# Performance work log

Hardware: AMD Instinct MI355X
Metric: run time of the kernel (lower is better)

## Reference

```python
import jax, jax.numpy as jnp
import numpy as np

EPS = 1e-5      # numerical floor for degrees / std / attenuation
LEAK = 0.01     # LeakyReLU slope of mixing FCLayer
AVG_D = 3.3     # log(avg_degree + 1) from init_kwargs
BIG = 1e30      # masking constant for max/min aggregators


def setup_inputs() -> dict:
    key = jax.random.key(0)
    ks = jax.random.split(key, 12)
    B, N, Din, De, H = 8, 256, 128, 64, 128
    s = 0.05
    inp = {
        "input": jax.random.normal(ks[0], (B, N, Din), jnp.float32),
        "adj": (jax.random.uniform(ks[1], (B, N, N)) < 0.1).astype(jnp.float32),
        "adj_features": jax.random.normal(ks[2], (B, N, N, De), jnp.float32),
        "hidden": jnp.zeros((B * N, H), jnp.float32),
        "pre_W": jax.random.normal(ks[3], (2 * Din + De, Din), jnp.float32) * s,
        "pre_b": jnp.zeros((Din,), jnp.float32),
        "post_W": jax.random.normal(ks[4], (13 * Din, H), jnp.float32) * s,
        "post_b": jnp.zeros((H,), jnp.float32),
        "mix_W": jax.random.normal(ks[5], (H, H), jnp.float32) * s,
        "mix_b": jnp.zeros((H,), jnp.float32),
        "gru_Wih": jax.random.normal(ks[6], (3 * H, H), jnp.float32) * s,
        "gru_Whh": jax.random.normal(ks[7], (3 * H, H), jnp.float32) * s,
    }
    return inp


def reference(input, adj, adj_features, hidden, pre_W, pre_b, post_W, post_b,
              mix_W, mix_b, gru_Wih, gru_Whh):
    B, N, Din = input.shape
    H = mix_W.shape[1]
    # --- pretrans MLP over all pairs: Linear([h_i, h_j, e_ij]) ---
    # split the weight into blocks so we never materialize h_cat (B,N,N,2Din+De)
    Wi, Wj, We = pre_W[:Din], pre_W[Din:2 * Din], pre_W[2 * Din:]
    hi = input @ Wi            # (B,N,Din)
    hj = input @ Wj            # (B,N,Din)
    h_mod = (hi[:, :, None, :] + hj[:, None, :, :]
             + jnp.einsum('bije,ek->bijk', adj_features, We) + pre_b)  # (B,N,N,Din)
    # --- multi-aggregator masked reduction over source axis j ---
    deg = jnp.sum(adj, axis=2)                       # (B,N)
    degc = jnp.maximum(deg, EPS)[..., None]          # (B,N,1)
    s1 = jnp.einsum('bij,bijk->bik', adj, h_mod)
    s2 = jnp.einsum('bij,bijk->bik', adj, h_mod * h_mod)
    mean = s1 / degc
    var = jnp.maximum(s2 / degc - mean * mean, 0.0)
    std = jnp.sqrt(var + EPS)
    mask = adj[..., None] > 0
    has_nb = (deg > 0)[..., None]
    mx = jnp.where(has_nb, jnp.max(jnp.where(mask, h_mod, -BIG), axis=2), 0.0)
    mn = jnp.where(has_nb, jnp.min(jnp.where(mask, h_mod, BIG), axis=2), 0.0)
    m = jnp.concatenate([mean, mx, mn, std], axis=2)  # (B,N,4*Din)
    # --- scalers: identity, amplification, attenuation ---
    slog = (jnp.log(deg + 1.0) / AVG_D)[..., None]    # (B,N,1)
    m = jnp.concatenate([m, m * slog, m / (slog + EPS)], axis=2)  # (B,N,12*Din)
    # --- posttrans Linear + mixing FCLayer (LeakyReLU) ---
    m_cat = jnp.concatenate([input, m], axis=2)       # (B,N,13*Din)
    y = m_cat @ post_W + post_b                       # (B,N,H)
    y = y @ mix_W + mix_b
    y = jnp.where(y > 0, y, LEAK * y)
    # --- GRUCell (bias=False), torch gate order r,z,n ---
    x = y.reshape(B * N, H)
    gi = x @ gru_Wih.T
    gh = hidden @ gru_Whh.T
    r = jax.nn.sigmoid(gi[:, :H] + gh[:, :H])
    z = jax.nn.sigmoid(gi[:, H:2 * H] + gh[:, H:2 * H])
    n = jnp.tanh(gi[:, 2 * H:] + r * gh[:, 2 * H:])
    h_new = (1.0 - z) * n + z * hidden
    return h_new.reshape(B, N, H)
```

## Files before the change

### kernel.cpp

```cpp
#include <hip/hip_runtime.h>
#include <cstdint>
#include <cstddef>

#define EPSF 1e-5f
#define LEAKF 0.01f
#define AVGD 3.3f

static constexpr int Nn = 256, DIN = 128, DE = 64, Hn = 128;
static constexpr int BN = 2048;
static constexpr int KP = 1664;
static constexpr int KM = 1536;

typedef short bf16x8 __attribute__((ext_vector_type(8)));
typedef float f32x4  __attribute__((ext_vector_type(4)));
union BF8 { bf16x8 v; uint16_t u[8]; };

__device__ __forceinline__ float bf2f(uint16_t u) { return __uint_as_float(((uint32_t)u) << 16); }
__device__ __forceinline__ float bflo(uint32_t u)  { return __uint_as_float(u << 16); }
__device__ __forceinline__ uint16_t f2bf(float f) {
  uint32_t u = __float_as_uint(f);
  u += 0x7fffu + ((u >> 16) & 1u);
  return (uint16_t)(u >> 16);
}

__device__ __forceinline__ int detect_bf16(const uint32_t* w) {
  float lo = bflo(w[threadIdx.x & 63]);
  unsigned long long ok = __ballot(fabsf(lo) < 64.f);
  return ok == 0xFFFFFFFFFFFFFFFFull;
}
__device__ __forceinline__ float loadf(const void* p, size_t i, int isbf) {
  return isbf ? bf2f(((const uint16_t*)p)[i]) : ((const float*)p)[i];
}
__device__ __forceinline__ bf16x8 load_a8(const void* p, size_t elem, int isbf) {
  if (isbf) return *(const bf16x8*)((const uint16_t*)p + elem);
  const float* s = (const float*)p + elem;
  BF8 r;
  #pragma unroll
  for (int e = 0; e < 8; e++) r.u[e] = f2bf(s[e]);
  return r.v;
}
__device__ __forceinline__ f32x4 mfma16(bf16x8 a, bf16x8 b, f32x4 c) {
  return __builtin_amdgcn_mfma_f32_16x16x32_bf16(a, b, c, 0, 0, 0);
}

__global__ __launch_bounds__(256) void k_prep1(
    const void* __restrict__ input, const void* __restrict__ pre_W,
    const void* __restrict__ pre_b, const void* __restrict__ post_W,
    const void* __restrict__ mix_W, const void* __restrict__ Wih,
    const void* __restrict__ Whh,
    uint16_t* __restrict__ postTb, uint16_t* __restrict__ mixTb,
    uint16_t* __restrict__ WeB, uint16_t* __restrict__ Wihb,
    uint16_t* __restrict__ Whhb,
    float* __restrict__ hi, float* __restrict__ hj) {
  __shared__ float tile[32][33];
  int isbf = detect_bf16((const uint32_t*)input);
  int b = blockIdx.x, tid = threadIdx.x;

  if (b >= 276) {
    int lane = tid & 63, w = tid >> 6;
    int wg = (b - 276) * 4 + w;
    int rt = wg >> 4, nt = wg & 15;
    int ishj = nt >> 3, ct = nt & 7;
    int m16 = lane & 15, quad = lane >> 4;
    int col = ct * 16 + m16;
    int row = rt * 16 + m16;
    int kbase = ishj ? 128 : 0;
    f32x4 acc = {0.f, 0.f, 0.f, 0.f};
    #pragma unroll
    for (int kt = 0; kt < 4; kt++) {
      bf16x8 a = load_a8(input, (size_t)row * 128 + kt * 32 + quad * 8, isbf);
      BF8 bb;
      #pragma unroll
      for (int j = 0; j < 8; j++)
        bb.u[j] = f2bf(loadf(pre_W, (size_t)(kbase + kt * 32 + quad * 8 + j) * 128 + col, isbf));
      acc = mfma16(a, bb.v, acc);
    }
    float bias = ishj ? 0.f : loadf(pre_b, col, isbf);
    float* dst = ishj ? hj : hi;
    #pragma unroll
    for (int r = 0; r < 4; r++)
      dst[(size_t)(rt * 16 + quad * 4 + r) * 128 + col] = acc[r] + bias;
    return;
  }

  if (b < 224) {
    const void* src; uint16_t* bdst; int R, t;
    if (b < 208) { src = post_W; bdst = postTb; R = KP;  t = b; }
    else         { src = mix_W;  bdst = mixTb;  R = 128; t = b - 208; }
    int bx = t & 3, by = t >> 2;
    int tx = tid & 31, ty = tid >> 5;
    int c0 = bx * 32, r0 = by * 32;
    #pragma unroll
    for (int dy = 0; dy < 32; dy += 8)
      tile[ty + dy][tx] = loadf(src, (size_t)(r0 + ty + dy) * 128 + (c0 + tx), isbf);
    __syncthreads();
    #pragma unroll
    for (int dy = 0; dy < 32; dy += 8)
      bdst[(size_t)(c0 + ty + dy) * R + (r0 + tx)] = f2bf(tile[tx][ty + dy]);
  } else {
    const void* src; uint16_t* dst; int base; size_t soff = 0;
    if (b < 228)      { src = pre_W; dst = WeB;  base = (b - 224) * 2048; soff = 256 * 128; }
    else if (b < 252) { src = Wih;   dst = Wihb; base = (b - 228) * 2048; }
    else              { src = Whh;   dst = Whhb; base = (b - 252) * 2048; }
    int i = base + tid * 8;
    uint16_t v[8];
    if (isbf) *(uint4*)v = *(const uint4*)((const uint16_t*)src + soff + i);
    else { const float* s = (const float*)src + soff + i;
           #pragma unroll
           for (int e = 0; e < 8; e++) v[e] = f2bf(s[e]); }
    *(uint4*)(dst + i) = *(uint4*)v;
  }
}

__global__ __launch_bounds__(256) void k2_mfma(
    const void* __restrict__ input, const void* __restrict__ adj_raw,
    const void* __restrict__ af_raw,
    const float* __restrict__ hi, const float* __restrict__ hj,
    const uint16_t* __restrict__ WeB, uint16_t* __restrict__ Mb) {
  __shared__ int s_cnt;
  __shared__ int nbr[Nn];
  __shared__ __align__(16) uint16_t A_lds[2][16 * 72];
  int isbf = detect_bf16((const uint32_t*)input);
  int bi = blockIdx.x, tid = threadIdx.x;
  if (tid == 0) s_cnt = 0;
  __syncthreads();
  {
    float a = loadf(adj_raw, (size_t)bi * Nn + tid, isbf);
    if (a > 0.f) nbr[atomicAdd(&s_cnt, 1)] = tid;
  }
  __syncthreads();
  int cnt = s_cnt;

  int lane = tid & 63, w = tid >> 6;
  int m16 = lane & 15, quad = lane >> 4;
  int col0 = w * 32 + m16, col1 = col0 + 16;

  BF8 b00, b01, b10, b11;
  #pragma unroll
  for (int j = 0; j < 8; j++) {
    int k0 = quad * 8 + j, k1 = k0 + 32;
    b00.u[j] = WeB[(size_t)k0 * 128 + col0];
    b01.u[j] = WeB[(size_t)k1 * 128 + col0];
    b10.u[j] = WeB[(size_t)k0 * 128 + col1];
    b11.u[j] = WeB[(size_t)k1 * 128 + col1];
  }
  float base0 = hi[(size_t)bi * 128 + col0];
  float base1 = hi[(size_t)bi * 128 + col1];
  const float* hjb = &hj[(size_t)(bi & ~(Nn - 1)) * 128];

  float s1a = 0.f, s2a = 0.f, mxa = -1e30f, mna = 1e30f;
  float s1b = 0.f, s2b = 0.f, mxb = -1e30f, mnb = 1e30f;

  auto stage = [&](int ce, int buf) {
    if (tid < 128) {
      int e = tid >> 3, seg = tid & 7;
      int ei = ce + e; if (ei >= cnt) ei = cnt - 1;
      int j = nbr[ei];
      uint16_t v[8];
      if (isbf)
        *(uint4*)v = *(const uint4*)((const uint16_t*)af_raw + ((size_t)bi * Nn + j) * DE + seg * 8);
      else {
        const float* s = (const float*)af_raw + ((size_t)bi * Nn + j) * DE + seg * 8;
        #pragma unroll
        for (int x = 0; x < 8; x++) v[x] = f2bf(s[x]);
      }
      *(uint4*)&A_lds[buf][e * 72 + seg * 8] = *(uint4*)v;
    }
  };

  if (cnt > 0) stage(0, 0);
  __syncthreads();

  for (int ce = 0; ce < cnt; ce += 16) {
    int cur = (ce >> 4) & 1;
    if (ce + 16 < cnt) stage(ce + 16, cur ^ 1);
    float hjv0[4], hjv1[4]; int vld[4];
    #pragma unroll
    for (int r = 0; r < 4; r++) {
      int e = ce + quad * 4 + r;
      vld[r] = (e < cnt);
      int j = nbr[vld[r] ? e : (cnt - 1)];
      hjv0[r] = hjb[(size_t)j * 128 + col0];
      hjv1[r] = hjb[(size_t)j * 128 + col1];
    }
    bf16x8 a0 = *(const bf16x8*)&A_lds[cur][m16 * 72 + quad * 8];
    bf16x8 a1 = *(const bf16x8*)&A_lds[cur][m16 * 72 + 32 + quad * 8];
    f32x4 C0 = {0.f,0.f,0.f,0.f}, C1 = C0;
    C0 = mfma16(a0, b00.v, C0); C0 = mfma16(a1, b01.v, C0);
    C1 = mfma16(a0, b10.v, C1); C1 = mfma16(a1, b11.v, C1);
    #pragma unroll
    for (int r = 0; r < 4; r++) {
      float h0 = base0 + hjv0[r] + C0[r];
      float h1 = base1 + hjv1[r] + C1[r];
      if (vld[r]) {
        s1a += h0; s2a += h0 * h0; mxa = fmaxf(mxa, h0); mna = fminf(mna, h0);
        s1b += h1; s2b += h1 * h1; mxb = fmaxf(mxb, h1); mnb = fminf(mnb, h1);
      }
    }
    __syncthreads();
  }

  #pragma unroll
  for (int off = 16; off <= 32; off <<= 1) {
    s1a += __shfl_xor(s1a, off); s2a += __shfl_xor(s2a, off);
    mxa = fmaxf(mxa, __shfl_xor(mxa, off)); mna = fminf(mna, __shfl_xor(mna, off));
    s1b += __shfl_xor(s1b, off); s2b += __shfl_xor(s2b, off);
    mxb = fmaxf(mxb, __shfl_xor(mxb, off)); mnb = fminf(mnb, __shfl_xor(mnb, off));
  }
  if (quad == 0) {
    float deg = (float)cnt, degc = fmaxf(deg, EPSF);
    float slog = logf(deg + 1.f) / AVGD;
    float inv  = 1.f / (slog + EPSF);
    uint16_t* mo = Mb + (size_t)bi * KM;
    #pragma unroll
    for (int t = 0; t < 2; t++) {
      float s1 = t ? s1b : s1a, s2 = t ? s2b : s2a;
      float mx = t ? mxb : mxa, mn = t ? mnb : mna;
      int col = t ? col1 : col0;
      float mean = s1 / degc;
      float var  = fmaxf(s2 / degc - mean * mean, 0.f);
      float stdv = sqrtf(var + EPSF);
      if (cnt == 0) { mx = 0.f; mn = 0.f; }
      mo[0*128+col]  = f2bf(mean);        mo[1*128+col]  = f2bf(mx);
      mo[2*128+col]  = f2bf(mn);          mo[3*128+col]  = f2bf(stdv);
      mo[4*128+col]  = f2bf(mean * slog); mo[5*128+col]  = f2bf(mx * slog);
      mo[6*128+col]  = f2bf(mn * slog);   mo[7*128+col]  = f2bf(stdv * slog);
      mo[8*128+col]  = f2bf(mean * inv);  mo[9*128+col]  = f2bf(mx * inv);
      mo[10*128+col] = f2bf(mn * inv);    mo[11*128+col] = f2bf(stdv * inv);
    }
  }
}

__global__ __launch_bounds__(512) void k3_fused(
    const void* __restrict__ input, const uint16_t* __restrict__ Mb,
    const uint16_t* __restrict__ postTb, const void* __restrict__ post_b,
    const uint16_t* __restrict__ mixTb, const void* __restrict__ mix_b,
    const uint16_t* __restrict__ Wihb, const uint16_t* __restrict__ Whhb,
    const void* __restrict__ hidden, void* __restrict__ out) {
  constexpr int SX = 136;
  __shared__ __align__(16) uint16_t y_s[16 * SX];
  __shared__ __align__(16) uint16_t x_s[16 * SX];
  __shared__ __align__(16) uint16_t hid_s[16 * SX];
  int isbf = detect_bf16((const uint32_t*)input);
  int tid = threadIdx.x;
  int n0 = blockIdx.x * 16;
  if (tid < 256) {
    int row = tid >> 4, c = (tid & 15) * 8;
    uint16_t v[8];
    if (isbf) *(uint4*)v = *(const uint4*)((const uint16_t*)hidden + (size_t)(n0 + row) * 128 + c);
    else { const float* s = (const float*)hidden + (size_t)(n0 + row) * 128 + c;
           #pragma unroll
           for (int e = 0; e < 8; e++) v[e] = f2bf(s[e]); }
    *(uint4*)&hid_s[row * SX + c] = *(uint4*)v;
  }
  int lane = tid & 63, w = tid >> 6;
  int m16 = lane & 15, quad = lane >> 4;
  int col = w * 16 + m16;

  f32x4 acc0 = {0.f,0.f,0.f,0.f}, acc1 = acc0;
  const uint16_t* bp = postTb + (size_t)col * KP + quad * 8;
  #pragma unroll
  for (int kt = 0; kt < 4; kt += 2) {
    bf16x8 a0 = load_a8(input, (size_t)(n0 + m16) * 128 + kt * 32 + quad * 8, isbf);
    bf16x8 a1 = load_a8(input, (size_t)(n0 + m16) * 128 + kt * 32 + 32 + quad * 8, isbf);
    acc0 = mfma16(a0, *(const bf16x8*)(bp + kt * 32), acc0);
    acc1 = mfma16(a1, *(const bf16x8*)(bp + kt * 32 + 32), acc1);
  }
  const uint16_t* mp  = Mb + (size_t)(n0 + m16) * KM + quad * 8;
  const uint16_t* bp2 = bp + 4 * 32;
  #pragma unroll 4
  for (int kt = 0; kt < 48; kt += 2) {
    bf16x8 a0 = *(const bf16x8*)(mp + kt * 32);
    bf16x8 a1 = *(const bf16x8*)(mp + kt * 32 + 32);
    acc0 = mfma16(a0, *(const bf16x8*)(bp2 + kt * 32), acc0);
    acc1 = mfma16(a1, *(const bf16x8*)(bp2 + kt * 32 + 32), acc1);
  }
  float pb = loadf(post_b, col, isbf);
  #pragma unroll
  for (int r = 0; r < 4; r++)
    y_s[(quad * 4 + r) * SX + col] = f2bf(acc0[r] + acc1[r] + pb);
  __syncthreads();

  f32x4 acc = {0.f,0.f,0.f,0.f};
  const uint16_t* ya = &y_s[m16 * SX + quad * 8];
  const uint16_t* mb = mixTb + (size_t)col * 128 + quad * 8;
  #pragma unroll
  for (int kt = 0; kt < 4; kt++)
    acc = mfma16(*(const bf16x8*)(ya + kt * 32), *(const bf16x8*)(mb + kt * 32), acc);
  float mbias = loadf(mix_b, col, isbf);
  #pragma unroll
  for (int r = 0; r < 4; r++) {
    float v = acc[r] + mbias; v = v > 0.f ? v : LEAKF * v;
    x_s[(quad * 4 + r) * SX + col] = f2bf(v);
  }
  __syncthreads();

  f32x4 gi[3], gh[3];
  #pragma unroll
  for (int q = 0; q < 3; q++) { gi[q] = {0.f,0.f,0.f,0.f}; gh[q] = {0.f,0.f,0.f,0.f}; }
  const uint16_t* xa = &x_s[m16 * SX + quad * 8];
  const uint16_t* ha = &hid_s[m16 * SX + quad * 8];
  #pragma unroll
  for (int kt = 0; kt < 4; kt++) {
    bf16x8 ax = *(const bf16x8*)(xa + kt * 32);
    bf16x8 ah = *(const bf16x8*)(ha + kt * 32);
    #pragma unroll
    for (int q = 0; q < 3; q++) {
      bf16x8 bi_ = *(const bf16x8*)&Wihb[(size_t)(q * 128 + col) * 128 + kt * 32 + quad * 8];
      bf16x8 bh_ = *(const bf16x8*)&Whhb[(size_t)(q * 128 + col) * 128 + kt * 32 + quad * 8];
      gi[q] = mfma16(ax, bi_, gi[q]);
      gh[q] = mfma16(ah, bh_, gh[q]);
    }
  }
  #pragma unroll
  for (int r = 0; r < 4; r++) {
    int row = quad * 4 + r;
    float rg = 1.f / (1.f + expf(-(gi[0][r] + gh[0][r])));
    float zg = 1.f / (1.f + expf(-(gi[1][r] + gh[1][r])));
    float ng = tanhf(gi[2][r] + rg * gh[2][r]);
    float hv = bf2f(hid_s[row * SX + col]);
    float res = (1.f - zg) * ng + zg * hv;
    size_t oi = (size_t)(n0 + row) * 128 + col;
    if (isbf) ((uint16_t*)out)[oi] = f2bf(res);
    else      ((float*)out)[oi]    = res;
  }
}

extern "C" void kernel_launch(void* const* d_in, const int* in_sizes, int n_in,
                              void* d_out, int out_size, void* d_ws, size_t ws_size,
                              hipStream_t stream) {
  const void* input  = d_in[0];
  const void* adj    = d_in[1];
  const void* af     = d_in[2];
  const void* hidden = d_in[3];
  const void* pre_W  = d_in[4];
  const void* pre_b  = d_in[5];
  const void* post_W = d_in[6];
  const void* post_b = d_in[7];
  const void* mix_W  = d_in[8];
  const void* mix_b  = d_in[9];
  const void* Wih    = d_in[10];
  const void* Whh    = d_in[11];

  float* ws = (float*)d_ws;
  float* hi = ws;
  float* hj = hi + 262144;
  uint16_t* postTb = (uint16_t*)(hj + 262144);
  uint16_t* mixTb  = postTb + 212992;
  uint16_t* WeB    = mixTb + 16384;
  uint16_t* Wihb   = WeB + 8192;
  uint16_t* Whhb   = Wihb + 49152;
  uint16_t* Mb     = Whhb + 49152;

  k_prep1<<<788, 256, 0, stream>>>(input, pre_W, pre_b, post_W, mix_W, Wih, Whh,
                                   postTb, mixTb, WeB, Wihb, Whhb, hi, hj);
  k2_mfma<<<BN, 256, 0, stream>>>(input, adj, af, hi, hj, WeB, Mb);
  k3_fused<<<128, 512, 0, stream>>>(input, Mb, postTb, post_b, mixTb, mix_b,
                                    Wihb, Whhb, hidden, d_out);
}
```

Before: 238.1 us.

## Fuse neighbor aggregation and posttrans/GRU into one kernel via LDS

```diff
diff --git a/kernel.cpp b/kernel.cpp
--- a/kernel.cpp
+++ b/kernel.cpp
@@ -112,166 +112,195 @@
   }
 }
 
-__global__ __launch_bounds__(256) void k2_mfma(
+__global__ __launch_bounds__(512) void k23_fused(
     const void* __restrict__ input, const void* __restrict__ adj_raw,
-    const void* __restrict__ af_raw,
-    const float* __restrict__ hi, const float* __restrict__ hj,
-    const uint16_t* __restrict__ WeB, uint16_t* __restrict__ Mb) {
-  __shared__ int s_cnt;
-  __shared__ int nbr[Nn];
-  __shared__ __align__(16) uint16_t A_lds[2][16 * 72];
-  int isbf = detect_bf16((const uint32_t*)input);
-  int bi = blockIdx.x, tid = threadIdx.x;
-  if (tid == 0) s_cnt = 0;
-  __syncthreads();
-  {
-    float a = loadf(adj_raw, (size_t)bi * Nn + tid, isbf);
-    if (a > 0.f) nbr[atomicAdd(&s_cnt, 1)] = tid;
-  }
-  __syncthreads();
-  int cnt = s_cnt;
-
-  int lane = tid & 63, w = tid >> 6;
-  int m16 = lane & 15, quad = lane >> 4;
-  int col0 = w * 32 + m16, col1 = col0 + 16;
-
-  BF8 b00, b01, b10, b11;
-  #pragma unroll
-  for (int j = 0; j < 8; j++) {
-    int k0 = quad * 8 + j, k1 = k0 + 32;
-    b00.u[j] = WeB[(size_t)k0 * 128 + col0];
-    b01.u[j] = WeB[(size_t)k1 * 128 + col0];
-    b10.u[j] = WeB[(size_t)k0 * 128 + col1];
-    b11.u[j] = WeB[(size_t)k1 * 128 + col1];
-  }
-  float base0 = hi[(size_t)bi * 128 + col0];
-  float base1 = hi[(size_t)bi * 128 + col1];
-  const float* hjb = &hj[(size_t)(bi & ~(Nn - 1)) * 128];
-
-  float s1a = 0.f, s2a = 0.f, mxa = -1e30f, mna = 1e30f;
-  float s1b = 0.f, s2b = 0.f, mxb = -1e30f, mnb = 1e30f;
-
-  auto stage = [&](int ce, int buf) {
-    if (tid < 128) {
-      int e = tid >> 3, seg = tid & 7;
-      int ei = ce + e; if (ei >= cnt) ei = cnt - 1;
-      int j = nbr[ei];
-      uint16_t v[8];
-      if (isbf)
-        *(uint4*)v = *(const uint4*)((const uint16_t*)af_raw + ((size_t)bi * Nn + j) * DE + seg * 8);
-      else {
-        const float* s = (const float*)af_raw + ((size_t)bi * Nn + j) * DE + seg * 8;
-        #pragma unroll
-        for (int x = 0; x < 8; x++) v[x] = f2bf(s[x]);
-      }
-      *(uint4*)&A_lds[buf][e * 72 + seg * 8] = *(uint4*)v;
-    }
-  };
-
-  if (cnt > 0) stage(0, 0);
-  __syncthreads();
-
-  for (int ce = 0; ce < cnt; ce += 16) {
-    int cur = (ce >> 4) & 1;
-    if (ce + 16 < cnt) stage(ce + 16, cur ^ 1);
-    float hjv0[4], hjv1[4]; int vld[4];
-    #pragma unroll
-    for (int r = 0; r < 4; r++) {
-      int e = ce + quad * 4 + r;
-      vld[r] = (e < cnt);
-      int j = nbr[vld[r] ? e : (cnt - 1)];
-      hjv0[r] = hjb[(size_t)j * 128 + col0];
-      hjv1[r] = hjb[(size_t)j * 128 + col1];
-    }
-    bf16x8 a0 = *(const bf16x8*)&A_lds[cur][m16 * 72 + quad * 8];
-    bf16x8 a1 = *(const bf16x8*)&A_lds[cur][m16 * 72 + 32 + quad * 8];
-    f32x4 C0 = {0.f,0.f,0.f,0.f}, C1 = C0;
-    C0 = mfma16(a0, b00.v, C0); C0 = mfma16(a1, b01.v, C0);
-    C1 = mfma16(a0, b10.v, C1); C1 = mfma16(a1, b11.v, C1);
-    #pragma unroll
-    for (int r = 0; r < 4; r++) {
-      float h0 = base0 + hjv0[r] + C0[r];
-      float h1 = base1 + hjv1[r] + C1[r];
-      if (vld[r]) {
-        s1a += h0; s2a += h0 * h0; mxa = fmaxf(mxa, h0); mna = fminf(mna, h0);
-        s1b += h1; s2b += h1 * h1; mxb = fmaxf(mxb, h1); mnb = fminf(mnb, h1);
-      }
-    }
-    __syncthreads();
-  }
-
-  #pragma unroll
-  for (int off = 16; off <= 32; off <<= 1) {
-    s1a += __shfl_xor(s1a, off); s2a += __shfl_xor(s2a, off);
-    mxa = fmaxf(mxa, __shfl_xor(mxa, off)); mna = fminf(mna, __shfl_xor(mna, off));
-    s1b += __shfl_xor(s1b, off); s2b += __shfl_xor(s2b, off);
-    mxb = fmaxf(mxb, __shfl_xor(mxb, off)); mnb = fminf(mnb, __shfl_xor(mnb, off));
-  }
-  if (quad == 0) {
-    float deg = (float)cnt, degc = fmaxf(deg, EPSF);
-    float slog = logf(deg + 1.f) / AVGD;
-    float inv  = 1.f / (slog + EPSF);
-    uint16_t* mo = Mb + (size_t)bi * KM;
-    #pragma unroll
-    for (int t = 0; t < 2; t++) {
-      float s1 = t ? s1b : s1a, s2 = t ? s2b : s2a;
-      float mx = t ? mxb : mxa, mn = t ? mnb : mna;
-      int col = t ? col1 : col0;
-      float mean = s1 / degc;
-      float var  = fmaxf(s2 / degc - mean * mean, 0.f);
-      float stdv = sqrtf(var + EPSF);
-      if (cnt == 0) { mx = 0.f; mn = 0.f; }
-      mo[0*128+col]  = f2bf(mean);        mo[1*128+col]  = f2bf(mx);
-      mo[2*128+col]  = f2bf(mn);          mo[3*128+col]  = f2bf(stdv);
-      mo[4*128+col]  = f2bf(mean * slog); mo[5*128+col]  = f2bf(mx * slog);
-      mo[6*128+col]  = f2bf(mn * slog);   mo[7*128+col]  = f2bf(stdv * slog);
-      mo[8*128+col]  = f2bf(mean * inv);  mo[9*128+col]  = f2bf(mx * inv);
-      mo[10*128+col] = f2bf(mn * inv);    mo[11*128+col] = f2bf(stdv * inv);
-    }
-  }
-}
-
-__global__ __launch_bounds__(512) void k3_fused(
-    const void* __restrict__ input, const uint16_t* __restrict__ Mb,
+    const void* __restrict__ af_raw, const float* __restrict__ hi,
+    const float* __restrict__ hj, const uint16_t* __restrict__ WeB,
     const uint16_t* __restrict__ postTb, const void* __restrict__ post_b,
     const uint16_t* __restrict__ mixTb, const void* __restrict__ mix_b,
     const uint16_t* __restrict__ Wihb, const uint16_t* __restrict__ Whhb,
     const void* __restrict__ hidden, void* __restrict__ out) {
   constexpr int SX = 136;
+  __shared__ __align__(16) uint16_t m_s[16 * KM];
+  __shared__ __align__(16) uint16_t A_lds[8][2][16 * 72];
+  __shared__ uint16_t nbr_s[8][Nn];
   __shared__ __align__(16) uint16_t y_s[16 * SX];
   __shared__ __align__(16) uint16_t x_s[16 * SX];
   __shared__ __align__(16) uint16_t hid_s[16 * SX];
+
   int isbf = detect_bf16((const uint32_t*)input);
   int tid = threadIdx.x;
-  int n0 = blockIdx.x * 16;
+  int n0 = blockIdx.x * 8;
+
+  {
+    uint4 z = {0, 0, 0, 0};
+    #pragma unroll
+    for (int i = 0; i < 3; i++)
+      *(uint4*)((char*)m_s + 24576 + (tid * 3 + i) * 16) = z;
+  }
   if (tid < 256) {
     int row = tid >> 4, c = (tid & 15) * 8;
+    int sr = n0 + row; if (sr > BN - 1) sr = BN - 1;
     uint16_t v[8];
-    if (isbf) *(uint4*)v = *(const uint4*)((const uint16_t*)hidden + (size_t)(n0 + row) * 128 + c);
-    else { const float* s = (const float*)hidden + (size_t)(n0 + row) * 128 + c;
+    if (isbf) *(uint4*)v = *(const uint4*)((const uint16_t*)hidden + (size_t)sr * 128 + c);
+    else { const float* s = (const float*)hidden + (size_t)sr * 128 + c;
            #pragma unroll
            for (int e = 0; e < 8; e++) v[e] = f2bf(s[e]); }
     *(uint4*)&hid_s[row * SX + c] = *(uint4*)v;
   }
+
   int lane = tid & 63, w = tid >> 6;
   int m16 = lane & 15, quad = lane >> 4;
+
+  {
+    int gnode = n0 + w;
+    int g = gnode >> 8, nl = gnode & 255;
+    int cnt = 0;
+    #pragma unroll
+    for (int g4 = 0; g4 < 4; g4++) {
+      float a = loadf(adj_raw, (size_t)gnode * Nn + g4 * 64 + lane, isbf);
+      unsigned long long mb = __ballot(a > 0.f);
+      unsigned long long below = lane ? (~0ull >> (64 - lane)) : 0ull;
+      int pos = cnt + __popcll(mb & below);
+      if (a > 0.f) nbr_s[w][pos] = (uint16_t)(g4 * 64 + lane);
+      cnt += __popcll(mb);
+    }
+
+    float hiv[8];
+    BF8 b0[8], b1[8];
+    #pragma unroll
+    for (int ct = 0; ct < 8; ct++) {
+      int col = ct * 16 + m16;
+      hiv[ct] = hi[(size_t)gnode * 128 + col];
+      #pragma unroll
+      for (int j = 0; j < 8; j++) {
+        b0[ct].u[j] = WeB[(size_t)(quad * 8 + j) * 128 + col];
+        b1[ct].u[j] = WeB[(size_t)(32 + quad * 8 + j) * 128 + col];
+      }
+    }
+    float s1[8], s2[8], mxv[8], mnv[8];
+    #pragma unroll
+    for (int ct = 0; ct < 8; ct++) { s1[ct] = 0.f; s2[ct] = 0.f; mxv[ct] = -1e30f; mnv[ct] = 1e30f; }
+
+    int e_ = lane >> 2, seg = lane & 3;
+    uint32_t cr[8], nr[8];
+    auto load_chunk = [&](int ce, uint32_t* d) {
+      int ei = ce + e_; if (ei >= cnt) ei = cnt - 1;
+      int j = nbr_s[w][ei];
+      size_t base = (((size_t)g * Nn + nl) * Nn + j) * DE + seg * 16;
+      if (isbf) {
+        *(uint4*)d       = *(const uint4*)((const uint16_t*)af_raw + base);
+        *(uint4*)(d + 4) = *(const uint4*)((const uint16_t*)af_raw + base + 8);
+      } else {
+        const float* s = (const float*)af_raw + base;
+        #pragma unroll
+        for (int x = 0; x < 8; x++)
+          d[x] = (uint32_t)f2bf(s[2 * x]) | ((uint32_t)f2bf(s[2 * x + 1]) << 16);
+      }
+    };
+
+    if (cnt > 0) load_chunk(0, cr);
+    for (int ce = 0; ce < cnt; ce += 16) {
+      int bf = (ce >> 4) & 1;
+      {
+        uint16_t* dst = &A_lds[w][bf][e_ * 72 + seg * 16];
+        *(uint4*)dst = *(uint4*)cr;
+        *(uint4*)(dst + 8) = *(uint4*)(cr + 4);
+      }
+      if (ce + 16 < cnt) load_chunk(ce + 16, nr);
+      int vld[4], jn[4];
+      #pragma unroll
+      for (int r = 0; r < 4; r++) {
+        int e = ce + quad * 4 + r;
+        vld[r] = (e < cnt);
+        jn[r] = nbr_s[w][vld[r] ? e : (cnt - 1)];
+      }
+      float hjv[4][8];
+      #pragma unroll
+      for (int r = 0; r < 4; r++) {
+        #pragma unroll
+        for (int ct = 0; ct < 8; ct++)
+          hjv[r][ct] = hj[((size_t)g * Nn + jn[r]) * 128 + ct * 16 + m16];
+      }
+      bf16x8 a0 = *(const bf16x8*)&A_lds[w][bf][m16 * 72 + quad * 8];
+      bf16x8 a1 = *(const bf16x8*)&A_lds[w][bf][m16 * 72 + 32 + quad * 8];
+      #pragma unroll
+      for (int ct = 0; ct < 8; ct++) {
+        f32x4 C = {0.f, 0.f, 0.f, 0.f};
+        C = mfma16(a0, b0[ct].v, C);
+        C = mfma16(a1, b1[ct].v, C);
+        #pragma unroll
+        for (int r = 0; r < 4; r++) {
+          if (vld[r]) {
+            float h = hiv[ct] + hjv[r][ct] + C[r];
+            s1[ct] += h; s2[ct] += h * h;
+            mxv[ct] = fmaxf(mxv[ct], h); mnv[ct] = fminf(mnv[ct], h);
+          }
+        }
+      }
+      #pragma unroll
+      for (int x = 0; x < 8; x++) cr[x] = nr[x];
+    }
+
+    #pragma unroll
+    for (int ct = 0; ct < 8; ct++) {
+      #pragma unroll
+      for (int off = 16; off <= 32; off <<= 1) {
+        s1[ct] += __shfl_xor(s1[ct], off);
+        s2[ct] += __shfl_xor(s2[ct], off);
+        mxv[ct] = fmaxf(mxv[ct], __shfl_xor(mxv[ct], off));
+        mnv[ct] = fminf(mnv[ct], __shfl_xor(mnv[ct], off));
+      }
+    }
+    if (quad == 0) {
+      float deg = (float)cnt, degc = fmaxf(deg, EPSF);
+      float slog = logf(deg + 1.f) / AVGD;
+      float inv  = 1.f / (slog + EPSF);
+      int row = w;
+      auto put = [&](int s, int col, float v) {
+        uint32_t off = (uint32_t)(row * (KM * 2) + (s * 128 + col) * 2);
+        off ^= (uint32_t)((row & 7) << 4);
+        *(uint16_t*)((char*)m_s + off) = f2bf(v);
+      };
+      #pragma unroll
+      for (int ct = 0; ct < 8; ct++) {
+        int col = ct * 16 + m16;
+        float mean = s1[ct] / degc;
+        float var  = fmaxf(s2[ct] / degc - mean * mean, 0.f);
+        float stdv = sqrtf(var + EPSF);
+        float mx = mxv[ct], mn = mnv[ct];
+        if (cnt == 0) { mx = 0.f; mn = 0.f; }
+        put(0, col, mean);        put(1, col, mx);
+        put(2, col, mn);          put(3, col, stdv);
+        put(4, col, mean * slog); put(5, col, mx * slog);
+        put(6, col, mn * slog);   put(7, col, stdv * slog);
+        put(8, col, mean * inv);  put(9, col, mx * inv);
+        put(10, col, mn * inv);   put(11, col, stdv * inv);
+      }
+    }
+  }
+  __syncthreads();
+
   int col = w * 16 + m16;
-
-  f32x4 acc0 = {0.f,0.f,0.f,0.f}, acc1 = acc0;
+  f32x4 acc0 = {0.f, 0.f, 0.f, 0.f}, acc1 = acc0;
   const uint16_t* bp = postTb + (size_t)col * KP + quad * 8;
+  int ar = n0 + m16; if (ar > BN - 1) ar = BN - 1;
   #pragma unroll
   for (int kt = 0; kt < 4; kt += 2) {
-    bf16x8 a0 = load_a8(input, (size_t)(n0 + m16) * 128 + kt * 32 + quad * 8, isbf);
-    bf16x8 a1 = load_a8(input, (size_t)(n0 + m16) * 128 + kt * 32 + 32 + quad * 8, isbf);
+    bf16x8 a0 = load_a8(input, (size_t)ar * 128 + kt * 32 + quad * 8, isbf);
+    bf16x8 a1 = load_a8(input, (size_t)ar * 128 + kt * 32 + 32 + quad * 8, isbf);
     acc0 = mfma16(a0, *(const bf16x8*)(bp + kt * 32), acc0);
     acc1 = mfma16(a1, *(const bf16x8*)(bp + kt * 32 + 32), acc1);
   }
-  const uint16_t* mp  = Mb + (size_t)(n0 + m16) * KM + quad * 8;
-  const uint16_t* bp2 = bp + 4 * 32;
+  const uint16_t* bp2 = bp + 128;
+  uint32_t mrb = (uint32_t)(m16 * (KM * 2));
+  uint32_t msw = (uint32_t)((m16 & 7) << 4);
   #pragma unroll 4
   for (int kt = 0; kt < 48; kt += 2) {
-    bf16x8 a0 = *(const bf16x8*)(mp + kt * 32);
-    bf16x8 a1 = *(const bf16x8*)(mp + kt * 32 + 32);
+    uint32_t o0 = (mrb + (kt * 32 + quad * 8) * 2) ^ msw;
+    uint32_t o1 = (mrb + (kt * 32 + 32 + quad * 8) * 2) ^ msw;
+    bf16x8 a0 = *(const bf16x8*)((const char*)m_s + o0);
+    bf16x8 a1 = *(const bf16x8*)((const char*)m_s + o1);
     acc0 = mfma16(a0, *(const bf16x8*)(bp2 + kt * 32), acc0);
     acc1 = mfma16(a1, *(const bf16x8*)(bp2 + kt * 32 + 32), acc1);
   }
@@ -281,7 +310,7 @@
     y_s[(quad * 4 + r) * SX + col] = f2bf(acc0[r] + acc1[r] + pb);
   __syncthreads();
 
-  f32x4 acc = {0.f,0.f,0.f,0.f};
+  f32x4 acc = {0.f, 0.f, 0.f, 0.f};
   const uint16_t* ya = &y_s[m16 * SX + quad * 8];
   const uint16_t* mb = mixTb + (size_t)col * 128 + quad * 8;
   #pragma unroll
@@ -315,14 +344,16 @@
   #pragma unroll
   for (int r = 0; r < 4; r++) {
     int row = quad * 4 + r;
-    float rg = 1.f / (1.f + expf(-(gi[0][r] + gh[0][r])));
-    float zg = 1.f / (1.f + expf(-(gi[1][r] + gh[1][r])));
-    float ng = tanhf(gi[2][r] + rg * gh[2][r]);
-    float hv = bf2f(hid_s[row * SX + col]);
-    float res = (1.f - zg) * ng + zg * hv;
-    size_t oi = (size_t)(n0 + row) * 128 + col;
-    if (isbf) ((uint16_t*)out)[oi] = f2bf(res);
-    else      ((float*)out)[oi]    = res;
+    if (row < 8) {
+      float rg = 1.f / (1.f + expf(-(gi[0][r] + gh[0][r])));
+      float zg = 1.f / (1.f + expf(-(gi[1][r] + gh[1][r])));
+      float ng = tanhf(gi[2][r] + rg * gh[2][r]);
+      float hv = bf2f(hid_s[row * SX + col]);
+      float res = (1.f - zg) * ng + zg * hv;
+      size_t oi = (size_t)(n0 + row) * 128 + col;
+      if (isbf) ((uint16_t*)out)[oi] = f2bf(res);
+      else      ((float*)out)[oi]    = res;
+    }
   }
 }
 
@@ -350,11 +381,10 @@
   uint16_t* WeB    = mixTb + 16384;
   uint16_t* Wihb   = WeB + 8192;
   uint16_t* Whhb   = Wihb + 49152;
-  uint16_t* Mb     = Whhb + 49152;
 
   k_prep1<<<788, 256, 0, stream>>>(input, pre_W, pre_b, post_W, mix_W, Wih, Whh,
                                    postTb, mixTb, WeB, Wihb, Whhb, hi, hj);
-  k2_mfma<<<BN, 256, 0, stream>>>(input, adj, af, hi, hj, WeB, Mb);
-  k3_fused<<<128, 512, 0, stream>>>(input, Mb, postTb, post_b, mixTb, mix_b,
-                                    Wihb, Whhb, hidden, d_out);
-}
+  k23_fused<<<BN / 8, 512, 0, stream>>>(input, adj, af, hi, hj, WeB,
+                                        postTb, post_b, mixTb, mix_b,
+                                        Wihb, Whhb, hidden, d_out);
+}
```

Result: faster. 227.5 us (-4.5%).
